# Performance work log

Hardware: AMD Instinct MI355X
Metric: run time of the kernel (lower is better)

## Reference

```python
import jax, jax.numpy as jnp
import numpy as np

L = 0.24          # lambda step size
K = 0.03          # exp(log 0.03), conductance scale used by forward
NITER = 500       # ctor Niter
DEPS = 0.1


def _g(x, k):
    # Perona-Malik conductance: 1 / (1 + |x^2| / k^2); x real so |x*x| == x*x
    return 1.0 / (1.0 + (x * x) / (k * k))


def setup_inputs() -> dict:
    key = jax.random.key(0)
    k1, k2 = jax.random.split(key)
    guide = jax.random.normal(k1, (2, 3, 512, 512), dtype=jnp.float32)
    initial = jax.random.uniform(k2, (2, 1, 512, 512), dtype=jnp.float32)
    return {"guide": guide, "initial": initial}


def reference(guide, initial):
    # shift branch (jit-safe): forward adds deps if initial.min() <= deps, subtracts at end
    shift = jnp.where(jnp.min(initial) <= DEPS, DEPS, 0.0).astype(initial.dtype)
    depth0 = initial + shift

    # conductance coefficients from guide (mean abs channel gradient), shapes:
    # cv: [B,1,H-1,W], ch: [B,1,H,W-1]
    cv = _g(jnp.mean(jnp.abs(guide[:, :, 1:, :] - guide[:, :, :-1, :]), axis=1, keepdims=True), K)
    ch = _g(jnp.mean(jnp.abs(guide[:, :, :, 1:] - guide[:, :, :, :-1]), axis=1, keepdims=True), K)

    def step(I, _):
        # both diffs computed from the same I (matches torch: dv, dh read before writes;
        # the in-place +/- updates commute, so functional adds give identical math)
        dv = I[:, :, 1:, :] - I[:, :, :-1, :]
        dh = I[:, :, :, 1:] - I[:, :, :, :-1]
        tv = L * cv * dv
        th = L * ch * dh
        I = I.at[:, :, 1:, :].add(-tv)
        I = I.at[:, :, :-1, :].add(tv)
        I = I.at[:, :, :, 1:].add(-th)
        I = I.at[:, :, :, :-1].add(th)
        return I, None

    depth, _ = jax.lax.scan(step, depth0, None, length=NITER)
    y_pred = depth - shift
    return (y_pred, cv, ch)
```

## Files before the change

### kernel.cpp

```cpp
#include <hip/hip_runtime.h>


#define HH 512
#define WW 512
#define NB 2
static constexpr float LAM   = 0.24f;
static constexpr float KCOND = 0.03f;
static constexpr float DEPS_ = 0.1f;
static constexpr int IMG      = HH * WW;
static constexpr int N_DEPTH  = NB * IMG;
static constexpr int CV_PER_B = (HH - 1) * WW;
static constexpr int CH_PER_B = HH * (WW - 1);
static constexpr int N_CV     = NB * CV_PER_B;
static constexpr int N_CH     = NB * CH_PER_B;

static constexpr int T_FUSE = 10, NSS = 50;
static constexpr int TILE_W = 64, TILE_H = 32;
static constexpr int HALO_X = 12, HALO_Y = 10;
static constexpr int RW = TILE_W + 2 * HALO_X;
static constexpr int RH = TILE_H + 2 * HALO_Y;
static constexpr int NQ_ROW = RW / 4;
static constexpr int NQUAD  = NQ_ROW * RH;
static constexpr int SSZ    = (RH + 2) * RW;

static constexpr int NT  = 512;
static constexpr int QPT = 3;
static constexpr int CVW = RW;
static constexpr int CV_SZ = (RH + 1) * CVW;
static constexpr int CHW = RW + 8;
static constexpr int CH_SZ = RH * CHW;
static constexpr int BLOB_BLK = CV_SZ + CH_SZ;

static constexpr int QPT_F = 5;

__device__ __forceinline__ unsigned fkey(float f) {
    unsigned u = __float_as_uint(f);
    return (u & 0x80000000u) ? ~u : (u | 0x80000000u);
}
__device__ __forceinline__ float kinv(unsigned k) {
    return __uint_as_float((k & 0x80000000u) ? (k & 0x7fffffffu) : ~k);
}

__global__ void init_key_kernel(unsigned* key) { *key = 0xFFFFFFFFu; }

__global__ void min_kernel(const float* __restrict__ x, unsigned* key) {
    float m = 3.4e38f;
    for (int idx = blockIdx.x * blockDim.x + threadIdx.x; idx < N_DEPTH;
         idx += gridDim.x * blockDim.x)
        m = fminf(m, x[idx]);
    for (int off = 32; off > 0; off >>= 1) m = fminf(m, __shfl_down(m, off, 64));
    __shared__ float sm[4];
    int lane = threadIdx.x & 63, wv = threadIdx.x >> 6;
    if (lane == 0) sm[wv] = m;
    __syncthreads();
    if (threadIdx.x == 0) {
        float mm = fminf(fminf(sm[0], sm[1]), fminf(sm[2], sm[3]));
        atomicMin(key, fkey(mm));
    }
}

__global__ void coeff_kernel(const float* __restrict__ g, float* __restrict__ cv,
                             float* __restrict__ chh) {
    int idx = blockIdx.x * blockDim.x + threadIdx.x;
    constexpr float kk = KCOND * KCOND;
    if (idx < N_CV) {
        int b = idx / CV_PER_B;
        int r = idx - b * CV_PER_B;
        int i = r >> 9, j = r & (WW - 1);
        const float* gb = g + b * 3 * IMG + i * WW + j;
        float s = 0.f;
#pragma unroll
        for (int c = 0; c < 3; ++c) s += fabsf(gb[c * IMG + WW] - gb[c * IMG]);
        float m = s / 3.0f;
        cv[idx] = 1.0f / (1.0f + (m * m) / kk);
    } else if (idx < N_CV + N_CH) {
        int t = idx - N_CV;
        int b = t / CH_PER_B;
        int r = t - b * CH_PER_B;
        int i = r / (WW - 1);
        int j = r - i * (WW - 1);
        const float* gb = g + b * 3 * IMG + i * WW + j;
        float s = 0.f;
#pragma unroll
        for (int c = 0; c < 3; ++c) s += fabsf(gb[c * IMG + 1] - gb[c * IMG]);
        float m = s / 3.0f;
        chh[t] = 1.0f / (1.0f + (m * m) / kk);
    }
}

__global__ __launch_bounds__(256) void prep_planes(const float* __restrict__ cv_g,
                                                   const float* __restrict__ ch_g,
                                                   float* __restrict__ blob) {
    const int blk = blockIdx.x;
    const int b   = blk >> 7, t = blk & 127;
    const int y0  = (t >> 3) * TILE_H;
    const int x0  = (t & 7) * TILE_W;
    const float* cvb = cv_g + b * CV_PER_B;
    const float* chb = ch_g + b * CH_PER_B;
    float* pv = blob + blk * BLOB_BLK;
    float* ph = pv + CV_SZ;
    for (int i = threadIdx.x; i < CV_SZ; i += 256) {
        int rr = i / CVW, x = i - rr * CVW;
        int gy = y0 - HALO_Y + rr, gx = x0 - HALO_X + x;
        bool ok = (rr >= 1) && (rr <= RH - 1) && (gy >= 1) && (gy <= HH - 1) &&
                  (gx >= 0) && (gx < WW);
        pv[i] = ok ? LAM * cvb[(gy - 1) * WW + gx] : 0.f;
    }
    for (int i = threadIdx.x; i < CH_SZ; i += 256) {
        int rr = i / CHW, xe = i - rr * CHW;
        int gy = y0 - HALO_Y + rr, gxe = x0 - HALO_X + xe;
        bool ok = (xe >= 1) && (xe <= RW - 1) && (gy >= 0) && (gy < HH) &&
                  (gxe >= 1) && (gxe < WW);
        ph[i] = ok ? LAM * chb[gy * (WW - 1) + (gxe - 1)] : 0.f;
    }
}

template <bool ADD_SHIFT, bool SUB_SHIFT>
__global__ __launch_bounds__(NT, 1) void step_fast(
    const float* __restrict__ src, float* __restrict__ dst,
    const float* __restrict__ blob, const unsigned* __restrict__ key) {
    __shared__ float sb[2][SSZ];
    const int blk = blockIdx.x;
    const int b   = blk >> 7, t = blk & 127;
    const int y0  = (t >> 3) * TILE_H;
    const int x0  = (t & 7) * TILE_W;
    const float* srcb = src + b * IMG;
    const float* pv   = blob + blk * BLOB_BLK;
    const float* ph   = pv + CV_SZ;

    float shift = 0.f;
    if (ADD_SHIFT || SUB_SHIFT) shift = (kinv(*key) <= DEPS_) ? DEPS_ : 0.f;
    const int tid = threadIdx.x;

    float v[QPT][4], cu[QPT][4], cd[QPT][4], chq[QPT][5];
    int   roff[QPT], goff[QPT];
    bool  is_int[QPT], in_img[QPT];

#pragma unroll
    for (int q = 0; q < QPT; ++q) {
        int qi   = tid + q * NT;
        bool act = qi < NQUAD;
        int qc   = act ? qi : 0;
        int r    = qc / NQ_ROW;
        int x    = (qc - r * NQ_ROW) * 4;
        roff[q]  = (r + 1) * RW + x;
        int gy = y0 - HALO_Y + r, gx = x0 - HALO_X + x;
        bool gy_in = (gy >= 0) && (gy < HH);
        in_img[q]  = act && gy_in && (gx >= 0) && (gx <= WW - 4);
        goff[q]    = in_img[q] ? (gy * WW + gx) : 0;
        is_int[q]  = act && (r >= HALO_Y) && (r < HALO_Y + TILE_H) &&
                     (x >= HALO_X) && (x < HALO_X + TILE_W);
        float4 a  = *reinterpret_cast<const float4*>(&pv[r * CVW + x]);
        float4 d  = *reinterpret_cast<const float4*>(&pv[(r + 1) * CVW + x]);
        float4 h  = *reinterpret_cast<const float4*>(&ph[r * CHW + x]);
        float  h4 = ph[r * CHW + x + 4];
        float am = act ? 1.f : 0.f;
        cu[q][0] = a.x * am; cu[q][1] = a.y * am; cu[q][2] = a.z * am; cu[q][3] = a.w * am;
        cd[q][0] = d.x * am; cd[q][1] = d.y * am; cd[q][2] = d.z * am; cd[q][3] = d.w * am;
        chq[q][0] = h.x * am; chq[q][1] = h.y * am; chq[q][2] = h.z * am;
        chq[q][3] = h.w * am; chq[q][4] = h4 * am;
        float4 tv = {0.f, 0.f, 0.f, 0.f};
        if (in_img[q]) tv = *reinterpret_cast<const float4*>(srcb + goff[q]);
        if (ADD_SHIFT && in_img[q]) {
            tv.x += shift; tv.y += shift; tv.z += shift; tv.w += shift;
        }
        v[q][0] = tv.x; v[q][1] = tv.y; v[q][2] = tv.z; v[q][3] = tv.w;
    }

    for (int i = tid; i < RW; i += NT) {
        sb[0][i] = 0.f; sb[0][(RH + 1) * RW + i] = 0.f;
        sb[1][i] = 0.f; sb[1][(RH + 1) * RW + i] = 0.f;
    }
#pragma unroll
    for (int q = 0; q < QPT; ++q)
        *reinterpret_cast<float4*>(&sb[0][roff[q]]) =
            float4{v[q][0], v[q][1], v[q][2], v[q][3]};
    __syncthreads();

    int cur = 0;
    for (int it = 0; it < T_FUSE; ++it) {
        float nv[QPT][4];
#pragma unroll
        for (int q = 0; q < QPT; ++q) {
            const float* s = sb[cur];
            float4 up = *reinterpret_cast<const float4*>(&s[roff[q] - RW]);
            float4 dn = *reinterpret_cast<const float4*>(&s[roff[q] + RW]);
            float  lf = s[roff[q] - 1];
            float  rt = s[roff[q] + 4];
            float c0 = v[q][0], c1 = v[q][1], c2 = v[q][2], c3 = v[q][3];
            nv[q][0] = c0 - cu[q][0] * (c0 - up.x) + cd[q][0] * (dn.x - c0)
                          - chq[q][0] * (c0 - lf) + chq[q][1] * (c1 - c0);
            nv[q][1] = c1 - cu[q][1] * (c1 - up.y) + cd[q][1] * (dn.y - c1)
                          - chq[q][1] * (c1 - c0) + chq[q][2] * (c2 - c1);
            nv[q][2] = c2 - cu[q][2] * (c2 - up.z) + cd[q][2] * (dn.z - c2)
                          - chq[q][2] * (c2 - c1) + chq[q][3] * (c3 - c2);
            nv[q][3] = c3 - cu[q][3] * (c3 - up.w) + cd[q][3] * (dn.w - c3)
                          - chq[q][3] * (c3 - c2) + chq[q][4] * (rt - c3);
        }
        int nxt = cur ^ 1;
#pragma unroll
        for (int q = 0; q < QPT; ++q) {
            *reinterpret_cast<float4*>(&sb[nxt][roff[q]]) =
                float4{nv[q][0], nv[q][1], nv[q][2], nv[q][3]};
            v[q][0] = nv[q][0]; v[q][1] = nv[q][1];
            v[q][2] = nv[q][2]; v[q][3] = nv[q][3];
        }
        cur = nxt;
        __syncthreads();
    }

    float* dstb = dst + b * IMG;
#pragma unroll
    for (int q = 0; q < QPT; ++q) {
        if (is_int[q]) {
            float4 o{v[q][0], v[q][1], v[q][2], v[q][3]};
            if (SUB_SHIFT) { o.x -= shift; o.y -= shift; o.z -= shift; o.w -= shift; }
            *reinterpret_cast<float4*>(dstb + goff[q]) = o;
        }
    }
}

template <bool ADD_SHIFT, bool SUB_SHIFT>
__global__ __launch_bounds__(256, 1) void step_fused(
    const float* __restrict__ src, float* __restrict__ dst,
    const float* __restrict__ cv_g, const float* __restrict__ ch_g,
    const unsigned* __restrict__ key) {
    __shared__ float sb[2][SSZ];
    const int blk = blockIdx.x;
    const int b = blk >> 7, t = blk & 127;
    const int y0 = (t >> 3) * TILE_H, x0 = (t & 7) * TILE_W;
    const float* cvb = cv_g + b * CV_PER_B;
    const float* chb = ch_g + b * CH_PER_B;
    const float* srcb = src + b * IMG;
    float* dstb = dst + b * IMG;
    float shift = 0.f;
    if (ADD_SHIFT || SUB_SHIFT) shift = (kinv(*key) <= DEPS_) ? DEPS_ : 0.f;
    const int tid = threadIdx.x;
    float v[QPT_F][4], cu[QPT_F][4], cd[QPT_F][4], chq[QPT_F][5];
    int roff[QPT_F], rr[QPT_F], xx[QPT_F];
    bool act[QPT_F];
#pragma unroll
    for (int q = 0; q < QPT_F; ++q) {
        int qi = tid + q * 256;
        act[q] = qi < NQUAD;
        int qc = act[q] ? qi : 0;
        int r = qc / NQ_ROW;
        int x = (qc - r * NQ_ROW) * 4;
        rr[q] = r; xx[q] = x;
        roff[q] = (r + 1) * RW + x;
        int gy = y0 - HALO_Y + r, gx = x0 - HALO_X + x;
        bool gy_in = (gy >= 0) && (gy < HH);
#pragma unroll
        for (int j = 0; j < 4; ++j) {
            int gxx = gx + j;
            bool gx_in = (gxx >= 0) && (gxx < WW);
            bool vin = act[q] && gy_in && gx_in;
            float val = vin ? srcb[gy * WW + gxx] : 0.f;
            if (ADD_SHIFT) val += shift;
            v[q][j] = vin ? val : 0.f;
            bool up_ok = act[q] && (r >= 1) && (gy >= 1) && (gy < HH) && gx_in;
            cu[q][j] = up_ok ? LAM * cvb[(gy - 1) * WW + gxx] : 0.f;
            bool dn_ok = act[q] && (r <= RH - 2) && (gy >= 0) && (gy < HH - 1) && gx_in;
            cd[q][j] = dn_ok ? LAM * cvb[gy * WW + gxx] : 0.f;
        }
#pragma unroll
        for (int jj = 0; jj < 5; ++jj) {
            int xe = x + jj, gxe = gx + jj;
            bool ok = act[q] && (xe >= 1) && (xe <= RW - 1) && gy_in &&
                      (gxe >= 1) && (gxe < WW);
            chq[q][jj] = ok ? LAM * chb[gy * (WW - 1) + (gxe - 1)] : 0.f;
        }
    }
    for (int i = tid; i < RW; i += 256) {
        sb[0][i] = 0.f; sb[0][(RH + 1) * RW + i] = 0.f;
        sb[1][i] = 0.f; sb[1][(RH + 1) * RW + i] = 0.f;
    }
#pragma unroll
    for (int q = 0; q < QPT_F; ++q)
        if (act[q])
            *reinterpret_cast<float4*>(&sb[0][roff[q]]) =
                float4{v[q][0], v[q][1], v[q][2], v[q][3]};
    __syncthreads();
    int cur = 0;
    for (int it = 0; it < T_FUSE; ++it) {
        float nv[QPT_F][4];
#pragma unroll
        for (int q = 0; q < QPT_F; ++q) {
            const float* s = sb[cur];
            float4 up = *reinterpret_cast<const float4*>(&s[roff[q] - RW]);
            float4 dn = *reinterpret_cast<const float4*>(&s[roff[q] + RW]);
            float lf = s[roff[q] - 1];
            float rt = s[roff[q] + 4];
            float c0 = v[q][0], c1 = v[q][1], c2 = v[q][2], c3 = v[q][3];
            nv[q][0] = c0 - cu[q][0] * (c0 - up.x) + cd[q][0] * (dn.x - c0)
                          - chq[q][0] * (c0 - lf) + chq[q][1] * (c1 - c0);
            nv[q][1] = c1 - cu[q][1] * (c1 - up.y) + cd[q][1] * (dn.y - c1)
                          - chq[q][1] * (c1 - c0) + chq[q][2] * (c2 - c1);
            nv[q][2] = c2 - cu[q][2] * (c2 - up.z) + cd[q][2] * (dn.z - c2)
                          - chq[q][2] * (c2 - c1) + chq[q][3] * (c3 - c2);
            nv[q][3] = c3 - cu[q][3] * (c3 - up.w) + cd[q][3] * (dn.w - c3)
                          - chq[q][3] * (c3 - c2) + chq[q][4] * (rt - c3);
        }
        int nxt = cur ^ 1;
#pragma unroll
        for (int q = 0; q < QPT_F; ++q) {
            if (act[q])
                *reinterpret_cast<float4*>(&sb[nxt][roff[q]]) =
                    float4{nv[q][0], nv[q][1], nv[q][2], nv[q][3]};
            v[q][0] = nv[q][0]; v[q][1] = nv[q][1];
            v[q][2] = nv[q][2]; v[q][3] = nv[q][3];
        }
        cur = nxt;
        __syncthreads();
    }
#pragma unroll
    for (int q = 0; q < QPT_F; ++q) {
        if (!act[q]) continue;
        int r = rr[q], x = xx[q];
        if (r >= HALO_Y && r < HALO_Y + TILE_H && x >= HALO_X && x < HALO_X + TILE_W) {
            int gy = y0 - HALO_Y + r, gx = x0 - HALO_X + x;
            float4 o{v[q][0], v[q][1], v[q][2], v[q][3]};
            if (SUB_SHIFT) { o.x -= shift; o.y -= shift; o.z -= shift; o.w -= shift; }
            *reinterpret_cast<float4*>(dstb + gy * WW + gx) = o;
        }
    }
}

extern "C" void kernel_launch(void* const* d_in, const int* in_sizes, int n_in,
                              void* d_out, int out_size, void* d_ws, size_t ws_size,
                              hipStream_t stream) {
    const float* guide   = (const float*)d_in[0];
    const float* initial = (const float*)d_in[1];
    float* out    = (float*)d_out;
    float* out_y  = out;
    float* out_cv = out + N_DEPTH;
    float* out_ch = out + N_DEPTH + N_CV;

    unsigned* key = (unsigned*)d_ws;
    float* wsf    = (float*)d_ws;
    float* bufA   = wsf + 64;
    float* bufB   = bufA + N_DEPTH;
    float* blob   = bufB + N_DEPTH;

    const size_t need = (size_t)(64 + 2 * N_DEPTH + 256 * BLOB_BLK) * 4;
    const bool fast = ws_size >= need;

    hipLaunchKernelGGL(init_key_kernel, dim3(1), dim3(1), 0, stream, key);
    hipLaunchKernelGGL(min_kernel, dim3(256), dim3(256), 0, stream, initial, key);

    int nco = N_CV + N_CH;
    hipLaunchKernelGGL(coeff_kernel, dim3((nco + 255) / 256), dim3(256), 0, stream,
                       guide, out_cv, out_ch);
    if (fast)
        hipLaunchKernelGGL(prep_planes, dim3(256), dim3(256), 0, stream,
                           out_cv, out_ch, blob);

    float* bufs[2] = {bufA, bufB};
    for (int k = 0; k < NSS; ++k) {
        const float* src = (k == 0) ? initial : bufs[(k + 1) & 1];
        float*       dst = (k == NSS - 1) ? out_y : bufs[k & 1];
        if (fast) {
            if (k == 0)
                hipLaunchKernelGGL((step_fast<true, false>), dim3(256), dim3(NT), 0,
                                   stream, src, dst, blob, key);
            else if (k == NSS - 1)
                hipLaunchKernelGGL((step_fast<false, true>), dim3(256), dim3(NT), 0,
                                   stream, src, dst, blob, key);
            else
                hipLaunchKernelGGL((step_fast<false, false>), dim3(256), dim3(NT), 0,
                                   stream, src, dst, blob, key);
        } else {
            if (k == 0)
                hipLaunchKernelGGL((step_fused<true, false>), dim3(256), dim3(256), 0,
                                   stream, src, dst, out_cv, out_ch, key);
            else if (k == NSS - 1)
                hipLaunchKernelGGL((step_fused<false, true>), dim3(256), dim3(256), 0,
                                   stream, src, dst, out_cv, out_ch, key);
            else
                hipLaunchKernelGGL((step_fused<false, false>), dim3(256), dim3(256), 0,
                                   stream, src, dst, out_cv, out_ch, key);
        }
    }
}
```

Before: 521.7 us.

## Register-block 4x4 pixel units per thread with edge-only LDS exchange

Each thread now owns a 4-row by 4-column block of pixels kept in registers instead of three separate 1x4 quads. Only the top and bottom rows and the left and right columns of each block go to shared memory, in a compact layout with transposed column buffers, so vertical neighbours inside the block come from registers. The aim is less LDS traffic per fused iteration and fewer threads (320 instead of 512). In exchange each thread holds more registers and does more work, and the shared-memory indexing for the edge buffers is more complex.

```diff
diff --git a/kernel.cpp b/kernel.cpp
--- a/kernel.cpp
+++ b/kernel.cpp
@@ -23,8 +23,21 @@
 static constexpr int NQUAD  = NQ_ROW * RH;
 static constexpr int SSZ    = (RH + 2) * RW;
 
-static constexpr int NT  = 512;
-static constexpr int QPT = 3;
+static constexpr int NU_ROW = RW / 4;
+static constexpr int NBAND  = RH / 4;
+static constexpr int NUNIT  = NU_ROW * NBAND;
+static constexpr int NTF    = 320;
+
+static constexpr int S_LDS     = 92;
+static constexpr int RROWS     = 2 * NBAND + 2;
+static constexpr int ROWS_SZ   = RROWS * S_LDS;
+static constexpr int TRASH_OFF = ROWS_SZ;
+static constexpr int TRASH_SZ  = 576;
+static constexpr int ECNT      = NUNIT + 2;
+static constexpr int LCOL_OFF  = TRASH_OFF + TRASH_SZ;
+static constexpr int RCOL_OFF  = LCOL_OFF + ECNT * 4;
+static constexpr int BUF_SZ    = RCOL_OFF + ECNT * 4;
+
 static constexpr int CVW = RW;
 static constexpr int CV_SZ = (RH + 1) * CVW;
 static constexpr int CHW = RW + 8;
@@ -116,10 +129,10 @@
 }
 
 template <bool ADD_SHIFT, bool SUB_SHIFT>
-__global__ __launch_bounds__(NT, 1) void step_fast(
+__global__ __launch_bounds__(NTF, 1) void step_fast(
     const float* __restrict__ src, float* __restrict__ dst,
     const float* __restrict__ blob, const unsigned* __restrict__ key) {
-    __shared__ float sb[2][SSZ];
+    __shared__ float sb[2][BUF_SZ];
     const int blk = blockIdx.x;
     const int b   = blk >> 7, t = blk & 127;
     const int y0  = (t >> 3) * TILE_H;
@@ -132,78 +145,132 @@
     if (ADD_SHIFT || SUB_SHIFT) shift = (kinv(*key) <= DEPS_) ? DEPS_ : 0.f;
     const int tid = threadIdx.x;
 
-    float v[QPT][4], cu[QPT][4], cd[QPT][4], chq[QPT][5];
-    int   roff[QPT], goff[QPT];
-    bool  is_int[QPT], in_img[QPT];
-
-#pragma unroll
-    for (int q = 0; q < QPT; ++q) {
-        int qi   = tid + q * NT;
-        bool act = qi < NQUAD;
-        int qc   = act ? qi : 0;
-        int r    = qc / NQ_ROW;
-        int x    = (qc - r * NQ_ROW) * 4;
-        roff[q]  = (r + 1) * RW + x;
-        int gy = y0 - HALO_Y + r, gx = x0 - HALO_X + x;
-        bool gy_in = (gy >= 0) && (gy < HH);
-        in_img[q]  = act && gy_in && (gx >= 0) && (gx <= WW - 4);
-        goff[q]    = in_img[q] ? (gy * WW + gx) : 0;
-        is_int[q]  = act && (r >= HALO_Y) && (r < HALO_Y + TILE_H) &&
-                     (x >= HALO_X) && (x < HALO_X + TILE_W);
-        float4 a  = *reinterpret_cast<const float4*>(&pv[r * CVW + x]);
-        float4 d  = *reinterpret_cast<const float4*>(&pv[(r + 1) * CVW + x]);
-        float4 h  = *reinterpret_cast<const float4*>(&ph[r * CHW + x]);
-        float  h4 = ph[r * CHW + x + 4];
-        float am = act ? 1.f : 0.f;
-        cu[q][0] = a.x * am; cu[q][1] = a.y * am; cu[q][2] = a.z * am; cu[q][3] = a.w * am;
-        cd[q][0] = d.x * am; cd[q][1] = d.y * am; cd[q][2] = d.z * am; cd[q][3] = d.w * am;
-        chq[q][0] = h.x * am; chq[q][1] = h.y * am; chq[q][2] = h.z * am;
-        chq[q][3] = h.w * am; chq[q][4] = h4 * am;
+    const bool act  = tid < NUNIT;
+    const int  uc   = act ? tid : 0;
+    const int  band = uc / NU_ROW;
+    const int  px   = uc - band * NU_ROW;
+    const int  x    = px * 4;
+    const int  r0   = band * 4;
+
+    const int ro_t   = (2 * band + 1) * S_LDS + x;
+    const int up_off = ro_t - S_LDS;
+    const int dn_off = ro_t + 2 * S_LDS;
+    const int e_lf   = RCOL_OFF + uc * 4;
+    const int e_rt   = LCOL_OFF + (uc + 2) * 4;
+    int w_t  = ro_t;
+    int w_b  = ro_t + S_LDS;
+    int e_wl = LCOL_OFF + (tid + 1) * 4;
+    int e_wr = RCOL_OFF + (tid + 1) * 4;
+    if (!act) {
+        int ts = TRASH_OFF + (tid - NUNIT) * 16;
+        w_t = ts; w_b = ts + 4; e_wl = ts + 8; e_wr = ts + 12;
+    }
+
+    const int gx    = x0 - HALO_X + x;
+    const bool gx_in = (gx >= 0) && (gx <= WW - 4);
+    const bool x_int = (x >= HALO_X) && (x < HALO_X + TILE_W);
+    int  goffr[4];
+    bool inr[4], isr[4];
+#pragma unroll
+    for (int i = 0; i < 4; ++i) {
+        int gy   = y0 - HALO_Y + r0 + i;
+        inr[i]   = act && gx_in && (gy >= 0) && (gy < HH);
+        goffr[i] = inr[i] ? (gy * WW + gx) : 0;
+        int rr   = r0 + i;
+        isr[i]   = act && x_int && (rr >= HALO_Y) && (rr < HALO_Y + TILE_H);
+    }
+
+    const float am = act ? 1.f : 0.f;
+    float cvv[5][4], hh[4][5];
+#pragma unroll
+    for (int i = 0; i < 5; ++i) {
+        float4 a = *reinterpret_cast<const float4*>(&pv[(r0 + i) * CVW + x]);
+        cvv[i][0] = a.x * am; cvv[i][1] = a.y * am;
+        cvv[i][2] = a.z * am; cvv[i][3] = a.w * am;
+    }
+#pragma unroll
+    for (int i = 0; i < 4; ++i) {
+        float4 u  = *reinterpret_cast<const float4*>(&ph[(r0 + i) * CHW + x]);
+        float  u4 = ph[(r0 + i) * CHW + x + 4];
+        hh[i][0] = u.x * am; hh[i][1] = u.y * am; hh[i][2] = u.z * am;
+        hh[i][3] = u.w * am; hh[i][4] = u4 * am;
+    }
+
+    float vv[4][4];
+#pragma unroll
+    for (int i = 0; i < 4; ++i) {
         float4 tv = {0.f, 0.f, 0.f, 0.f};
-        if (in_img[q]) tv = *reinterpret_cast<const float4*>(srcb + goff[q]);
-        if (ADD_SHIFT && in_img[q]) {
+        if (inr[i]) tv = *reinterpret_cast<const float4*>(srcb + goffr[i]);
+        if (ADD_SHIFT && inr[i]) {
             tv.x += shift; tv.y += shift; tv.z += shift; tv.w += shift;
         }
-        v[q][0] = tv.x; v[q][1] = tv.y; v[q][2] = tv.z; v[q][3] = tv.w;
-    }
-
-    for (int i = tid; i < RW; i += NT) {
-        sb[0][i] = 0.f; sb[0][(RH + 1) * RW + i] = 0.f;
-        sb[1][i] = 0.f; sb[1][(RH + 1) * RW + i] = 0.f;
-    }
-#pragma unroll
-    for (int q = 0; q < QPT; ++q)
-        *reinterpret_cast<float4*>(&sb[0][roff[q]]) =
-            float4{v[q][0], v[q][1], v[q][2], v[q][3]};
+        vv[i][0] = tv.x; vv[i][1] = tv.y; vv[i][2] = tv.z; vv[i][3] = tv.w;
+    }
+
+    for (int i = tid; i < S_LDS; i += NTF) {
+        sb[0][i] = 0.f; sb[0][(RROWS - 1) * S_LDS + i] = 0.f;
+        sb[1][i] = 0.f; sb[1][(RROWS - 1) * S_LDS + i] = 0.f;
+    }
+    if (tid == 0) {
+        float4 z{0.f, 0.f, 0.f, 0.f};
+        *reinterpret_cast<float4*>(&sb[0][LCOL_OFF]) = z;
+        *reinterpret_cast<float4*>(&sb[1][LCOL_OFF]) = z;
+        *reinterpret_cast<float4*>(&sb[0][LCOL_OFF + (ECNT - 1) * 4]) = z;
+        *reinterpret_cast<float4*>(&sb[1][LCOL_OFF + (ECNT - 1) * 4]) = z;
+        *reinterpret_cast<float4*>(&sb[0][RCOL_OFF]) = z;
+        *reinterpret_cast<float4*>(&sb[1][RCOL_OFF]) = z;
+        *reinterpret_cast<float4*>(&sb[0][RCOL_OFF + (ECNT - 1) * 4]) = z;
+        *reinterpret_cast<float4*>(&sb[1][RCOL_OFF + (ECNT - 1) * 4]) = z;
+    }
+    *reinterpret_cast<float4*>(&sb[0][w_t])  = float4{vv[0][0], vv[0][1], vv[0][2], vv[0][3]};
+    *reinterpret_cast<float4*>(&sb[0][w_b])  = float4{vv[3][0], vv[3][1], vv[3][2], vv[3][3]};
+    *reinterpret_cast<float4*>(&sb[0][e_wl]) = float4{vv[0][0], vv[1][0], vv[2][0], vv[3][0]};
+    *reinterpret_cast<float4*>(&sb[0][e_wr]) = float4{vv[0][3], vv[1][3], vv[2][3], vv[3][3]};
     __syncthreads();
 
     int cur = 0;
     for (int it = 0; it < T_FUSE; ++it) {
-        float nv[QPT][4];
-#pragma unroll
-        for (int q = 0; q < QPT; ++q) {
-            const float* s = sb[cur];
-            float4 up = *reinterpret_cast<const float4*>(&s[roff[q] - RW]);
-            float4 dn = *reinterpret_cast<const float4*>(&s[roff[q] + RW]);
-            float  lf = s[roff[q] - 1];
-            float  rt = s[roff[q] + 4];
-            float c0 = v[q][0], c1 = v[q][1], c2 = v[q][2], c3 = v[q][3];
-            nv[q][0] = c0 - cu[q][0] * (c0 - up.x) + cd[q][0] * (dn.x - c0)
-                          - chq[q][0] * (c0 - lf) + chq[q][1] * (c1 - c0);
-            nv[q][1] = c1 - cu[q][1] * (c1 - up.y) + cd[q][1] * (dn.y - c1)
-                          - chq[q][1] * (c1 - c0) + chq[q][2] * (c2 - c1);
-            nv[q][2] = c2 - cu[q][2] * (c2 - up.z) + cd[q][2] * (dn.z - c2)
-                          - chq[q][2] * (c2 - c1) + chq[q][3] * (c3 - c2);
-            nv[q][3] = c3 - cu[q][3] * (c3 - up.w) + cd[q][3] * (dn.w - c3)
-                          - chq[q][3] * (c3 - c2) + chq[q][4] * (rt - c3);
-        }
+        const float* s = sb[cur];
+        float4 up4 = *reinterpret_cast<const float4*>(&s[up_off]);
+        float4 dn4 = *reinterpret_cast<const float4*>(&s[dn_off]);
+        float4 lf4 = *reinterpret_cast<const float4*>(&s[e_lf]);
+        float4 rt4 = *reinterpret_cast<const float4*>(&s[e_rt]);
+        const float upa[4] = {up4.x, up4.y, up4.z, up4.w};
+        const float dna[4] = {dn4.x, dn4.y, dn4.z, dn4.w};
+        const float lfa[4] = {lf4.x, lf4.y, lf4.z, lf4.w};
+        const float rta[4] = {rt4.x, rt4.y, rt4.z, rt4.w};
+
+        float nn[4][4];
+#pragma unroll
+        for (int i = 0; i < 4; ++i) {
+            const float u0 = (i == 0) ? upa[0] : vv[i - 1][0];
+            const float u1 = (i == 0) ? upa[1] : vv[i - 1][1];
+            const float u2 = (i == 0) ? upa[2] : vv[i - 1][2];
+            const float u3 = (i == 0) ? upa[3] : vv[i - 1][3];
+            const float d0 = (i == 3) ? dna[0] : vv[i + 1 > 3 ? 3 : i + 1][0];
+            const float d1 = (i == 3) ? dna[1] : vv[i + 1 > 3 ? 3 : i + 1][1];
+            const float d2 = (i == 3) ? dna[2] : vv[i + 1 > 3 ? 3 : i + 1][2];
+            const float d3 = (i == 3) ? dna[3] : vv[i + 1 > 3 ? 3 : i + 1][3];
+            nn[i][0] = vv[i][0] - cvv[i][0] * (vv[i][0] - u0) + cvv[i + 1][0] * (d0 - vv[i][0])
+                               - hh[i][0] * (vv[i][0] - lfa[i]) + hh[i][1] * (vv[i][1] - vv[i][0]);
+            nn[i][1] = vv[i][1] - cvv[i][1] * (vv[i][1] - u1) + cvv[i + 1][1] * (d1 - vv[i][1])
+                               - hh[i][1] * (vv[i][1] - vv[i][0]) + hh[i][2] * (vv[i][2] - vv[i][1]);
+            nn[i][2] = vv[i][2] - cvv[i][2] * (vv[i][2] - u2) + cvv[i + 1][2] * (d2 - vv[i][2])
+                               - hh[i][2] * (vv[i][2] - vv[i][1]) + hh[i][3] * (vv[i][3] - vv[i][2]);
+            nn[i][3] = vv[i][3] - cvv[i][3] * (vv[i][3] - u3) + cvv[i + 1][3] * (d3 - vv[i][3])
+                               - hh[i][3] * (vv[i][3] - vv[i][2]) + hh[i][4] * (rta[i] - vv[i][3]);
+        }
+
         int nxt = cur ^ 1;
-#pragma unroll
-        for (int q = 0; q < QPT; ++q) {
-            *reinterpret_cast<float4*>(&sb[nxt][roff[q]]) =
-                float4{nv[q][0], nv[q][1], nv[q][2], nv[q][3]};
-            v[q][0] = nv[q][0]; v[q][1] = nv[q][1];
-            v[q][2] = nv[q][2]; v[q][3] = nv[q][3];
+        float* d = sb[nxt];
+        *reinterpret_cast<float4*>(&d[w_t])  = float4{nn[0][0], nn[0][1], nn[0][2], nn[0][3]};
+        *reinterpret_cast<float4*>(&d[w_b])  = float4{nn[3][0], nn[3][1], nn[3][2], nn[3][3]};
+        *reinterpret_cast<float4*>(&d[e_wl]) = float4{nn[0][0], nn[1][0], nn[2][0], nn[3][0]};
+        *reinterpret_cast<float4*>(&d[e_wr]) = float4{nn[0][3], nn[1][3], nn[2][3], nn[3][3]};
+#pragma unroll
+        for (int i = 0; i < 4; ++i) {
+            vv[i][0] = nn[i][0]; vv[i][1] = nn[i][1];
+            vv[i][2] = nn[i][2]; vv[i][3] = nn[i][3];
         }
         cur = nxt;
         __syncthreads();
@@ -211,11 +278,11 @@
 
     float* dstb = dst + b * IMG;
 #pragma unroll
-    for (int q = 0; q < QPT; ++q) {
-        if (is_int[q]) {
-            float4 o{v[q][0], v[q][1], v[q][2], v[q][3]};
+    for (int i = 0; i < 4; ++i) {
+        if (isr[i]) {
+            float4 o{vv[i][0], vv[i][1], vv[i][2], vv[i][3]};
             if (SUB_SHIFT) { o.x -= shift; o.y -= shift; o.z -= shift; o.w -= shift; }
-            *reinterpret_cast<float4*>(dstb + goff[q]) = o;
+            *reinterpret_cast<float4*>(dstb + goffr[i]) = o;
         }
     }
 }
@@ -361,13 +428,13 @@
         float*       dst = (k == NSS - 1) ? out_y : bufs[k & 1];
         if (fast) {
             if (k == 0)
-                hipLaunchKernelGGL((step_fast<true, false>), dim3(256), dim3(NT), 0,
+                hipLaunchKernelGGL((step_fast<true, false>), dim3(256), dim3(NTF), 0,
                                    stream, src, dst, blob, key);
             else if (k == NSS - 1)
-                hipLaunchKernelGGL((step_fast<false, true>), dim3(256), dim3(NT), 0,
+                hipLaunchKernelGGL((step_fast<false, true>), dim3(256), dim3(NTF), 0,
                                    stream, src, dst, blob, key);
             else
-                hipLaunchKernelGGL((step_fast<false, false>), dim3(256), dim3(NT), 0,
+                hipLaunchKernelGGL((step_fast<false, false>), dim3(256), dim3(NTF), 0,
                                    stream, src, dst, blob, key);
         } else {
             if (k == 0)
```

Result: slower. 571.3 us (+9.5%).
